# Kernel tuning notes

Measured on AMD Instinct MI355X. Metric: run time of the kernel, lower is better.

The kernel has to match this reference:

```python
import jax, jax.numpy as jnp
import numpy as np

DT = 1.0
TOL = 2e-4
MAX_FK = 0.1


def _lap(x):
    # 5-point Laplacian with periodic boundary (roll-based), x: [B,1,H,W]
    return (jnp.roll(x, 1, -1) + jnp.roll(x, -1, -1)
            + jnp.roll(x, 1, -2) + jnp.roll(x, -1, -2) - 4.0 * x)


def _gs_step(u, v, Du, Dv, F, k, dt):
    uvv = u * v * v
    u_next = u + dt * (Du * _lap(u) - uvv + F * (1.0 - u))
    v_next = v + dt * (Dv * _lap(v) + uvv - (F + k) * v)
    return u_next, v_next


def setup_inputs() -> dict:
    key = jax.random.key(0)
    k1, k2 = jax.random.split(key)
    B, H, W = 32, 512, 512
    # physically sensible Gray-Scott init: u near 1, v small
    u = 1.0 - 0.5 * jax.random.uniform(k1, (B, 1, H, W), dtype=jnp.float32)
    v = 0.25 * jax.random.uniform(k2, (B, 1, H, W), dtype=jnp.float32)
    return {
        "u": u,
        "v": v,
        "log_Du": jnp.float32(-2.0),
        "log_Dv": jnp.float32(-2.0),
        "raw_F": jnp.float32(0.0),
        "raw_k": jnp.float32(0.0),
        "max_steps": 64,
        "K": 32,
    }


def reference(u, v, log_Du, log_Dv, raw_F, raw_k, max_steps, K):
    # params_tensor()
    Du = jax.nn.softplus(log_Du)
    Dv = jax.nn.softplus(log_Dv)
    F = MAX_FK * jax.nn.sigmoid(raw_F)
    k = MAX_FK * jax.nn.sigmoid(raw_k)

    B = u.shape[0]
    converged0 = jnp.zeros((B,), dtype=bool)

    # Phase 1: simulate-until-converged (per-sample freeze), expressed as a
    # fixed-length masked scan (no data-dependent shapes). Samples that were
    # already converged at the start of a step keep their state frozen,
    # matching the index_select/scatter semantics of the torch loop.
    def steady_body(carry, _):
        u, v, conv = carry
        u_next, v_next = _gs_step(u, v, Du, Dv, F, k, DT)
        du = jnp.max(jnp.abs(u_next - u), axis=(1, 2, 3))
        dv = jnp.max(jnp.abs(v_next - v), axis=(1, 2, 3))
        newly = jnp.maximum(du, dv) < TOL
        m = conv[:, None, None, None]
        u2 = jnp.where(m, u, u_next)
        v2 = jnp.where(m, v, v_next)
        return (u2, v2, conv | newly), None

    (u, v, converged), _ = jax.lax.scan(
        steady_body, (u, v, converged0), None, length=max_steps)

    # Phase 2: K differentiable steps (trunc BPTT segment), no masking
    def bptt_body(carry, _):
        u, v = carry
        return _gs_step(u, v, Du, Dv, F, k, DT), None

    (u, v), _ = jax.lax.scan(bptt_body, (u, v), None, length=K)
    return (u, v)
```

## Files before the change

### kernel.cpp

```cpp
#include <hip/hip_runtime.h>

#define HH 512
#define WW 512
#define BB 32
#define NIMG (HH * WW)
#define NT (BB * NIMG)
#define TOLF 0.0002f
#define HS 32
#define NSTRIP (HH / HS)
#define TRP 16
#define TIP (TRP + 2)
#define NTBP (HH / TRP)

__device__ __forceinline__ void gs_math(
    const float4& cu, const float4& uu, const float4& ud, float ul, float ur,
    const float4& cv, const float4& vu, const float4& vd, float vl, float vr,
    float Du, float Dv, float F, float Fk, float4& un, float4& vn)
{
    float4 lu, lv;
    lu.x = ul   + cu.y + uu.x + ud.x - 4.f * cu.x;
    lu.y = cu.x + cu.z + uu.y + ud.y - 4.f * cu.y;
    lu.z = cu.y + cu.w + uu.z + ud.z - 4.f * cu.z;
    lu.w = cu.z + ur   + uu.w + ud.w - 4.f * cu.w;
    lv.x = vl   + cv.y + vu.x + vd.x - 4.f * cv.x;
    lv.y = cv.x + cv.z + vu.y + vd.y - 4.f * cv.y;
    lv.z = cv.y + cv.w + vu.z + vd.z - 4.f * cv.z;
    lv.w = cv.z + vr   + vu.w + vd.w - 4.f * cv.w;
    float uvv;
    uvv  = cu.x * cv.x * cv.x;
    un.x = cu.x + (Du * lu.x - uvv + F * (1.f - cu.x));
    vn.x = cv.x + (Dv * lv.x + uvv - Fk * cv.x);
    uvv  = cu.y * cv.y * cv.y;
    un.y = cu.y + (Du * lu.y - uvv + F * (1.f - cu.y));
    vn.y = cv.y + (Dv * lv.y + uvv - Fk * cv.y);
    uvv  = cu.z * cv.z * cv.z;
    un.z = cu.z + (Du * lu.z - uvv + F * (1.f - cu.z));
    vn.z = cv.z + (Dv * lv.z + uvv - Fk * cv.z);
    uvv  = cu.w * cv.w * cv.w;
    un.w = cu.w + (Du * lu.w - uvv + F * (1.f - cu.w));
    vn.w = cv.w + (Dv * lv.w + uvv - Fk * cv.w);
}

__device__ __forceinline__ void load_row(const float* __restrict__ s,
                                         int base, int baseUp, int baseDn, int c0,
                                         float4& c, float4& up, float4& dn, float& l, float& r)
{
    c  = *(const float4*)(s + base   + c0);
    up = *(const float4*)(s + baseUp + c0);
    dn = *(const float4*)(s + baseDn + c0);
    l  = s[base + ((c0 - 1) & (WW - 1))];
    r  = s[base + ((c0 + 4) & (WW - 1))];
}

__device__ __forceinline__ float dmax8(const float4& un, const float4& cu,
                                       const float4& vn, const float4& cv)
{
    return fmaxf(
        fmaxf(fmaxf(fabsf(un.x - cu.x), fabsf(un.y - cu.y)),
              fmaxf(fabsf(un.z - cu.z), fabsf(un.w - cu.w))),
        fmaxf(fmaxf(fabsf(vn.x - cv.x), fabsf(vn.y - cv.y)),
              fmaxf(fabsf(vn.z - cv.z), fabsf(vn.w - cv.w))));
}

__global__ __launch_bounds__(512)
void gs_quad(const float* __restrict__ fsU, const float* __restrict__ fsV,
             float* wsU, float* wsV, float* outU, float* outV,
             const float* __restrict__ consts,
             const int* __restrict__ conv, const int* __restrict__ par,
             float* __restrict__ pmax, int tpar, int steady)
{
    __shared__ float ring[3][2][4][WW];
    __shared__ float sred[8];

    const int b = blockIdx.y;
    if (steady && conv[b]) return;
    const int p = par[b] ^ tpar;
    const float* __restrict__ su = p ? outU : wsU;
    const float* __restrict__ sv = p ? outV : wsV;
    float* __restrict__ dU = p ? wsU : outU;
    float* __restrict__ dV = p ? wsV : outV;
    if (fsU) { su = fsU; sv = fsV; }

    const float Du = consts[0], Dv = consts[1], F = consts[2], Fk = consts[3];
    const int t = threadIdx.x;
    const int g = t >> 7;
    const int gt = t & 127;
    const int lane = t & 63;
    const int c0 = gt * 4;
    const int R0 = blockIdx.x * HS;
    const size_t ib = (size_t)b * NIMG;

    const int readStart = 4 * g;
    const int readEnd   = 39 + 2 * g;
    float4 m0u = {0,0,0,0}, m1u = {0,0,0,0}, m2u = {0,0,0,0};
    float4 m0v = {0,0,0,0}, m1v = {0,0,0,0}, m2v = {0,0,0,0};
    float dm = 0.f;

    for (int j = 0; j <= 46; ++j) {
        float4 nu = {0,0,0,0}, nv = {0,0,0,0};
        if (j >= readStart && j <= readEnd) {
            const int rr = j - 4 - 3 * g;
            if (g == 0) {
                const int gr = (R0 + rr) & (HH - 1);
                nu = *(const float4*)(su + ib + (size_t)gr * WW + c0);
                nv = *(const float4*)(sv + ib + (size_t)gr * WW + c0);
            } else {
                const int s = rr & 3;
                nu = *(const float4*)&ring[g - 1][0][s][c0];
                nv = *(const float4*)&ring[g - 1][1][s][c0];
            }
        }

        if (j >= readStart + 3 && j <= readEnd + 1) {
            const int rp = j - 6 - 3 * g;
            float ul = __shfl_up(m1u.w, 1),   vl = __shfl_up(m1v.w, 1);
            float ur = __shfl_down(m1u.x, 1), vr = __shfl_down(m1v.x, 1);
            if (lane == 0 || lane == 63) {
                if (g == 0) {
                    const int gr = (R0 + rp) & (HH - 1);
                    const size_t rb = ib + (size_t)gr * WW;
                    if (lane == 0) { ul = su[rb + ((c0 - 1) & (WW - 1))];
                                     vl = sv[rb + ((c0 - 1) & (WW - 1))]; }
                    else           { ur = su[rb + ((c0 + 4) & (WW - 1))];
                                     vr = sv[rb + ((c0 + 4) & (WW - 1))]; }
                } else {
                    const int s = rp & 3;
                    if (lane == 0) { ul = ring[g - 1][0][s][(c0 - 1) & (WW - 1)];
                                     vl = ring[g - 1][1][s][(c0 - 1) & (WW - 1)]; }
                    else           { ur = ring[g - 1][0][s][(c0 + 4) & (WW - 1)];
                                     vr = ring[g - 1][1][s][(c0 + 4) & (WW - 1)]; }
                }
            }
            float4 un, vn;
            gs_math(m1u, m0u, m2u, ul, ur, m1v, m0v, m2v, vl, vr, Du, Dv, F, Fk, un, vn);
            if (g == 3) {
                *(float4*)(dU + ib + (size_t)(R0 + rp) * WW + c0) = un;
                *(float4*)(dV + ib + (size_t)(R0 + rp) * WW + c0) = vn;
            } else {
                const int s = rp & 3;
                *(float4*)&ring[g][0][s][c0] = un;
                *(float4*)&ring[g][1][s][c0] = vn;
            }
            if (steady && rp >= 0 && rp < HS)
                dm = fmaxf(dm, dmax8(un, m1u, vn, m1v));
        }

        m0u = m1u; m1u = m2u; m2u = nu;
        m0v = m1v; m1v = m2v; m2v = nv;
        __syncthreads();
    }

    if (steady) {
        #pragma unroll
        for (int off = 1; off < 64; off <<= 1)
            dm = fmaxf(dm, __shfl_xor(dm, off));
        const int w = t >> 6;
        if (lane == 0) sred[w] = dm;
        __syncthreads();
        if (gt == 0) {
            const int idx = b * NSTRIP + blockIdx.x;
            pmax[g * BB * NSTRIP + idx] = fmaxf(sred[2 * g], sred[2 * g + 1]);
        }
    }
}

__global__ void gs_upd(const int* __restrict__ convO, const int* __restrict__ parO,
                       int* convN, int* parN, int* rbJ,
                       const float* __restrict__ pmax)
{
    const int b = blockIdx.x, t = threadIdx.x;
    if (convO[b]) { if (t == 0) { convN[b] = 1; parN[b] = parO[b]; rbJ[b] = 0; } return; }
    float v0 = 0.f, v1 = 0.f, v2 = 0.f, v3 = 0.f;
    if (t < NSTRIP) {
        const int idx = b * NSTRIP + t;
        v0 = pmax[0 * BB * NSTRIP + idx];
        v1 = pmax[1 * BB * NSTRIP + idx];
        v2 = pmax[2 * BB * NSTRIP + idx];
        v3 = pmax[3 * BB * NSTRIP + idx];
    }
    #pragma unroll
    for (int off = 1; off < NSTRIP; off <<= 1) {
        v0 = fmaxf(v0, __shfl_xor(v0, off));
        v1 = fmaxf(v1, __shfl_xor(v1, off));
        v2 = fmaxf(v2, __shfl_xor(v2, off));
        v3 = fmaxf(v3, __shfl_xor(v3, off));
    }
    if (t == 0) {
        int j = 0;
        if      (v0 < TOLF) j = 1;
        else if (v1 < TOLF) j = 2;
        else if (v2 < TOLF) j = 3;
        else if (v3 < TOLF) j = 4;
        const int pO = parO[b];
        convN[b] = (j != 0);
        parN[b]  = (j == 3) ? pO : (pO ^ 1);
        rbJ[b]   = (j >= 1 && j <= 3) ? j : 0;
    }
}

__global__ __launch_bounds__(256)
void gs_rollA(const float* __restrict__ fsU, const float* __restrict__ fsV,
              float* wsU, float* wsV, float* outU, float* outV,
              const float* __restrict__ consts,
              const int* __restrict__ parO, const int* __restrict__ rbJ)
{
    __shared__ float iu[TIP][WW];
    __shared__ float iv[TIP][WW];
    const int b = blockIdx.y;
    if (rbJ[b] < 2) return;
    const int p = parO[b];
    const float* __restrict__ su = p ? outU : wsU;
    const float* __restrict__ sv = p ? outV : wsV;
    float* __restrict__ dU = p ? wsU : outU;
    float* __restrict__ dV = p ? wsV : outV;
    if (fsU) { su = fsU; sv = fsV; }
    const float Du = consts[0], Dv = consts[1], F = consts[2], Fk = consts[3];
    const int t = threadIdx.x, c0 = (t & 127) * 4, rw = t >> 7;
    const int r0 = blockIdx.x * TRP;
    for (int i = 0; i < TIP; i += 2) {
        const int li = i + rw;
        const int h  = (r0 - 1 + li) & (HH - 1);
        const int hm = (h - 1) & (HH - 1);
        const int hp = (h + 1) & (HH - 1);
        const int base   = b * NIMG + h  * WW;
        const int baseUp = b * NIMG + hm * WW;
        const int baseDn = b * NIMG + hp * WW;
        float4 cu, uu, ud, cv, vu, vd; float ul, ur, vl, vr;
        load_row(su, base, baseUp, baseDn, c0, cu, uu, ud, ul, ur);
        load_row(sv, base, baseUp, baseDn, c0, cv, vu, vd, vl, vr);
        float4 un, vn;
        gs_math(cu, uu, ud, ul, ur, cv, vu, vd, vl, vr, Du, Dv, F, Fk, un, vn);
        *(float4*)(&iu[li][c0]) = un;
        *(float4*)(&iv[li][c0]) = vn;
    }
    __syncthreads();
    for (int i = 0; i < TRP; i += 2) {
        const int li = 1 + i + rw;
        const int h  = r0 + i + rw;
        float4 cu = *(const float4*)(&iu[li][c0]);
        float4 uu = *(const float4*)(&iu[li - 1][c0]);
        float4 ud = *(const float4*)(&iu[li + 1][c0]);
        const float ul = iu[li][(c0 - 1) & (WW - 1)];
        const float ur = iu[li][(c0 + 4) & (WW - 1)];
        float4 cv = *(const float4*)(&iv[li][c0]);
        float4 vu = *(const float4*)(&iv[li - 1][c0]);
        float4 vd = *(const float4*)(&iv[li + 1][c0]);
        const float vl = iv[li][(c0 - 1) & (WW - 1)];
        const float vr = iv[li][(c0 + 4) & (WW - 1)];
        float4 un, vn;
        gs_math(cu, uu, ud, ul, ur, cv, vu, vd, vl, vr, Du, Dv, F, Fk, un, vn);
        *(float4*)(dU + b * NIMG + h * WW + c0) = un;
        *(float4*)(dV + b * NIMG + h * WW + c0) = vn;
    }
}

__global__ __launch_bounds__(256)
void gs_rollB(const float* __restrict__ fsU, const float* __restrict__ fsV,
              float* wsU, float* wsV, float* outU, float* outV,
              const float* __restrict__ consts,
              const int* __restrict__ parO, const int* __restrict__ rbJ)
{
    const int b = blockIdx.y;
    const int j = rbJ[b];
    if (j != 1 && j != 3) return;
    const int q = parO[b] ^ (j == 3 ? 1 : 0);
    const float* __restrict__ su = q ? outU : wsU;
    const float* __restrict__ sv = q ? outV : wsV;
    float* __restrict__ dU = q ? wsU : outU;
    float* __restrict__ dV = q ? wsV : outV;
    if (j == 1 && fsU) { su = fsU; sv = fsV; }
    const float Du = consts[0], Dv = consts[1], F = consts[2], Fk = consts[3];
    const int idx = blockIdx.x * 256 + threadIdx.x;
    const int h  = idx >> 7;
    const int c0 = (idx & 127) * 4;
    const int hm = (h - 1) & (HH - 1);
    const int hp = (h + 1) & (HH - 1);
    const int base   = b * NIMG + h  * WW;
    const int baseUp = b * NIMG + hm * WW;
    const int baseDn = b * NIMG + hp * WW;
    float4 cu, uu, ud, cv, vu, vd; float ul, ur, vl, vr;
    load_row(su, base, baseUp, baseDn, c0, cu, uu, ud, ul, ur);
    load_row(sv, base, baseUp, baseDn, c0, cv, vu, vd, vl, vr);
    float4 un, vn;
    gs_math(cu, uu, ud, ul, ur, cv, vu, vd, vl, vr, Du, Dv, F, Fk, un, vn);
    *(float4*)(dU + base + c0) = un;
    *(float4*)(dV + base + c0) = vn;
}

__global__ void gs_init(const float* lDu, const float* lDv, const float* rF, const float* rk,
                        float* consts, int* conv0, int* par0, int* rbJ)
{
    const int t = threadIdx.x;
    if (t == 0) {
        const float a = lDu[0], c = lDv[0];
        const float Du = (a > 0.f) ? a + log1pf(expf(-a)) : log1pf(expf(a));
        const float Dv = (c > 0.f) ? c + log1pf(expf(-c)) : log1pf(expf(c));
        const float F  = 0.1f / (1.f + expf(-rF[0]));
        const float kk = 0.1f / (1.f + expf(-rk[0]));
        consts[0] = Du; consts[1] = Dv; consts[2] = F; consts[3] = F + kk;
    }
    if (t < BB) { conv0[t] = 0; par0[t] = 0; rbJ[t] = 0; }
}

__launch_bounds__(256)
__global__ void gs_final(const float* __restrict__ wsU, const float* __restrict__ wsV,
                         float* outU, float* outV, const int* __restrict__ par)
{
    const int b = blockIdx.y;
    if (par[b] != 0) return;
    const int off = b * NIMG + (blockIdx.x * 256 + threadIdx.x) * 4;
    *(float4*)(outU + off) = *(const float4*)(wsU + off);
    *(float4*)(outV + off) = *(const float4*)(wsV + off);
}

extern "C" void kernel_launch(void* const* d_in, const int* in_sizes, int n_in,
                              void* d_out, int out_size, void* d_ws, size_t ws_size,
                              hipStream_t stream)
{
    const float* in_u = (const float*)d_in[0];
    const float* in_v = (const float*)d_in[1];
    const float* lDu  = (const float*)d_in[2];
    const float* lDv  = (const float*)d_in[3];
    const float* rF   = (const float*)d_in[4];
    const float* rk   = (const float*)d_in[5];
    const int NQUAD_STEADY = 16;
    const int NQUAD_BPTT   = 8;

    float* wsU = (float*)d_ws;
    float* wsV = wsU + NT;
    float* aux = wsV + NT;
    float* consts = aux;
    int* conv0 = (int*)(aux + 4);
    int* par0  = conv0 + BB;
    int* conv1 = par0 + BB;
    int* par1  = conv1 + BB;
    int* rbJ   = par1 + BB;
    float* pmax = (float*)(rbJ + BB);

    float* outU = (float*)d_out;
    float* outV = outU + NT;

    gs_init<<<1, 64, 0, stream>>>(lDu, lDv, rF, rk, consts, conv0, par0, rbJ);

    const dim3 gridQ(NSTRIP, BB);
    for (int s = 0; s < NQUAD_STEADY; ++s) {
        int* cO = (s & 1) ? conv1 : conv0;
        int* pO = (s & 1) ? par1  : par0;
        int* cN = (s & 1) ? conv0 : conv1;
        int* pN = (s & 1) ? par0  : par1;
        const float* fU = (s == 0) ? in_u : nullptr;
        const float* fV = (s == 0) ? in_v : nullptr;
        gs_quad<<<gridQ, 512, 0, stream>>>(fU, fV, wsU, wsV, outU, outV, consts,
                                           cO, pO, pmax, 0, 1);
        gs_upd<<<BB, 64, 0, stream>>>(cO, pO, cN, pN, rbJ, pmax);
        gs_rollA<<<dim3(NTBP, BB), 256, 0, stream>>>(fU, fV, wsU, wsV, outU, outV,
                                                     consts, pO, rbJ);
        gs_rollB<<<dim3(NIMG / 1024, BB), 256, 0, stream>>>(fU, fV, wsU, wsV, outU, outV,
                                                            consts, pO, rbJ);
    }
    for (int j = 0; j < NQUAD_BPTT; ++j) {
        gs_quad<<<gridQ, 512, 0, stream>>>(nullptr, nullptr, wsU, wsV, outU, outV, consts,
                                           conv0, par0, pmax, j & 1, 0);
    }
    gs_final<<<dim3(NIMG / 1024, BB), 256, 0, stream>>>(wsU, wsV, outU, outV, par0);
}
```

Before: 1.309 ms.

## Prefetch global rows two iterations ahead and exchange wave-edge halos via shared memory

The first group of four stages now keeps a two-row register queue of global loads issued two iterations early, so global latency overlaps with compute across the barrier-synchronized pipeline. Left and right halo values at wave boundaries are published to small shared arrays from the loaded rows, replacing scattered scalar global loads by lanes 0 and 63. This adds register pressure and extra shared writes, and relies on the wave pairing (wv^1) covering the periodic wrap across the 128-thread row.

```diff
diff --git a/kernel.cpp b/kernel.cpp
--- a/kernel.cpp
+++ b/kernel.cpp
@@ -70,6 +70,8 @@
              float* __restrict__ pmax, int tpar, int steady)
 {
     __shared__ float ring[3][2][4][WW];
+    __shared__ float eXu[2][4], eXv[2][4];
+    __shared__ float eWu[2][4], eWv[2][4];
     __shared__ float sred[8];
 
     const int b = blockIdx.y;
@@ -86,6 +88,7 @@
     const int g = t >> 7;
     const int gt = t & 127;
     const int lane = t & 63;
+    const int wv = (t >> 6) & 1;
     const int c0 = gt * 4;
     const int R0 = blockIdx.x * HS;
     const size_t ib = (size_t)b * NIMG;
@@ -94,42 +97,47 @@
     const int readEnd   = 39 + 2 * g;
     float4 m0u = {0,0,0,0}, m1u = {0,0,0,0}, m2u = {0,0,0,0};
     float4 m0v = {0,0,0,0}, m1v = {0,0,0,0}, m2v = {0,0,0,0};
+    float4 q0u = {0,0,0,0}, q0v = {0,0,0,0}, q1u = {0,0,0,0}, q1v = {0,0,0,0};
     float dm = 0.f;
+
+    if (g == 0) {
+        const int g0 = (R0 - 4) & (HH - 1);
+        const int g1 = (R0 - 3) & (HH - 1);
+        q0u = *(const float4*)(su + ib + (size_t)g0 * WW + c0);
+        q0v = *(const float4*)(sv + ib + (size_t)g0 * WW + c0);
+        q1u = *(const float4*)(su + ib + (size_t)g1 * WW + c0);
+        q1v = *(const float4*)(sv + ib + (size_t)g1 * WW + c0);
+    }
 
     for (int j = 0; j <= 46; ++j) {
         float4 nu = {0,0,0,0}, nv = {0,0,0,0};
-        if (j >= readStart && j <= readEnd) {
-            const int rr = j - 4 - 3 * g;
-            if (g == 0) {
-                const int gr = (R0 + rr) & (HH - 1);
+        if (g == 0) {
+            if (j <= 37) {
+                const int gr = (R0 + j - 2) & (HH - 1);
                 nu = *(const float4*)(su + ib + (size_t)gr * WW + c0);
                 nv = *(const float4*)(sv + ib + (size_t)gr * WW + c0);
-            } else {
-                const int s = rr & 3;
-                nu = *(const float4*)&ring[g - 1][0][s][c0];
-                nv = *(const float4*)&ring[g - 1][1][s][c0];
             }
+        } else if (j >= readStart && j <= readEnd) {
+            const int rr = j - 4 - 3 * g;
+            const int s = rr & 3;
+            nu = *(const float4*)&ring[g - 1][0][s][c0];
+            nv = *(const float4*)&ring[g - 1][1][s][c0];
         }
 
         if (j >= readStart + 3 && j <= readEnd + 1) {
             const int rp = j - 6 - 3 * g;
             float ul = __shfl_up(m1u.w, 1),   vl = __shfl_up(m1v.w, 1);
             float ur = __shfl_down(m1u.x, 1), vr = __shfl_down(m1v.x, 1);
-            if (lane == 0 || lane == 63) {
-                if (g == 0) {
-                    const int gr = (R0 + rp) & (HH - 1);
-                    const size_t rb = ib + (size_t)gr * WW;
-                    if (lane == 0) { ul = su[rb + ((c0 - 1) & (WW - 1))];
-                                     vl = sv[rb + ((c0 - 1) & (WW - 1))]; }
-                    else           { ur = su[rb + ((c0 + 4) & (WW - 1))];
-                                     vr = sv[rb + ((c0 + 4) & (WW - 1))]; }
-                } else {
-                    const int s = rp & 3;
-                    if (lane == 0) { ul = ring[g - 1][0][s][(c0 - 1) & (WW - 1)];
-                                     vl = ring[g - 1][1][s][(c0 - 1) & (WW - 1)]; }
-                    else           { ur = ring[g - 1][0][s][(c0 + 4) & (WW - 1)];
-                                     vr = ring[g - 1][1][s][(c0 + 4) & (WW - 1)]; }
-                }
+            if (g == 0) {
+                const int es = rp & 3;
+                if (lane == 0)  { ul = eWu[wv ^ 1][es]; vl = eWv[wv ^ 1][es]; }
+                if (lane == 63) { ur = eXu[wv ^ 1][es]; vr = eXv[wv ^ 1][es]; }
+            } else if (lane == 0 || lane == 63) {
+                const int s = rp & 3;
+                if (lane == 0) { ul = ring[g - 1][0][s][(c0 - 1) & (WW - 1)];
+                                 vl = ring[g - 1][1][s][(c0 - 1) & (WW - 1)]; }
+                else           { ur = ring[g - 1][0][s][(c0 + 4) & (WW - 1)];
+                                 vr = ring[g - 1][1][s][(c0 + 4) & (WW - 1)]; }
             }
             float4 un, vn;
             gs_math(m1u, m0u, m2u, ul, ur, m1v, m0v, m2v, vl, vr, Du, Dv, F, Fk, un, vn);
@@ -145,8 +153,19 @@
                 dm = fmaxf(dm, dmax8(un, m1u, vn, m1v));
         }
 
-        m0u = m1u; m1u = m2u; m2u = nu;
-        m0v = m1v; m1v = m2v; m2v = nv;
+        if (g == 0) {
+            if (j <= 39) {
+                const int sl = (j - 4) & 3;
+                if (lane == 0)  { eXu[wv][sl] = q0u.x; eXv[wv][sl] = q0v.x; }
+                if (lane == 63) { eWu[wv][sl] = q0u.w; eWv[wv][sl] = q0v.w; }
+            }
+            m0u = m1u; m1u = m2u; m2u = q0u;
+            m0v = m1v; m1v = m2v; m2v = q0v;
+            q0u = q1u; q0v = q1v; q1u = nu; q1v = nv;
+        } else {
+            m0u = m1u; m1u = m2u; m2u = nu;
+            m0v = m1v; m1v = m2v; m2v = nv;
+        }
         __syncthreads();
     }
 
```

Result: slower. 1.386 ms (+5.9%).
